# Kernel tuning notes

Hardware: AMD Instinct MI355X
Metric: run time of the kernel (lower is better)

The kernel has to match this reference:

```python
import jax, jax.numpy as jnp
import numpy as np

EVENT_DIM = 128   # event vocabulary
HIDDEN = 256      # 2*128 bilstm output
EMB = 16          # event embedding size
TMP = 128         # tmp_dim
T = 65536         # timesteps
NEG_SLOPE = 0.01  # torch leaky_relu default


def setup_inputs() -> dict:
    key = jax.random.key(0)
    ks = jax.random.split(key, 4)
    return {
        "output": jax.random.normal(ks[0], (T, 1, HIDDEN), dtype=jnp.float32),
        "event_index": 0,  # event_index['NONE']
        "emb_table": jax.random.normal(ks[1], (EVENT_DIM, EMB), dtype=jnp.float32) * 0.02,
        "W1": jax.random.normal(ks[2], (HIDDEN + EMB, TMP), dtype=jnp.float32) / np.sqrt(HIDDEN + EMB).astype(np.float32),
        "b1": jnp.zeros((TMP,), dtype=jnp.float32),
        "W2": jax.random.normal(ks[3], (TMP, EVENT_DIM), dtype=jnp.float32) / np.sqrt(TMP).astype(np.float32),
        "b2": jnp.zeros((EVENT_DIM,), dtype=jnp.float32),
    }


def reference(output, event_index, emb_table, W1, b1, W2, b2):
    # output: [T, 1, HIDDEN]; dropout is identity in eval/inference mode.
    x = output[:, 0, :]  # [T, HIDDEN]

    def step(idx, xt):
        ev = emb_table[idx]                       # [EMB] embedding of previous prediction
        inp = jnp.concatenate([xt, ev], axis=0)   # [HIDDEN+EMB]
        h = jax.nn.leaky_relu(inp @ W1 + b1, negative_slope=NEG_SLOPE)
        logp = jax.nn.log_softmax(h @ W2 + b2)    # [EVENT_DIM]
        nidx = jnp.argmax(logp)                   # greedy feedback (infer=True)
        return nidx, (logp, emb_table[nidx], nidx)

    init = jnp.asarray(event_index, dtype=jnp.int32)
    _, (ner_output, ner_emb, ner_index) = jax.lax.scan(step, init, x)
    # ner_output: [T, EVENT_DIM]; ner_emb: [T, 1, EMB]; ner_index: [T]
    return ner_output, ner_emb[:, None, :], ner_index
```

## Files before the change

### kernel.cpp

```cpp
#include <hip/hip_runtime.h>

#define TT   65536
#define HID  256
#define EMBD 16
#define TMPD 128
#define ED   128
#define TAU  5e-4f
#define EPS  1e-3f
#define NEGINF (-3.402823466e38f)
#define TPB  32
#define CAPW (1u << 20)
#define CMAX 24

typedef __bf16 bf16x8 __attribute__((ext_vector_type(8)));
typedef float  f32x4  __attribute__((ext_vector_type(4)));
typedef short  s16x8  __attribute__((ext_vector_type(8)));

__device__ inline unsigned short f2bf(float f) {
    __bf16 b = (__bf16)f;
    return __builtin_bit_cast(unsigned short, b);
}
__device__ inline float bf2f(unsigned short u) {
    unsigned int x = ((unsigned int)u) << 16;
    return __builtin_bit_cast(float, x);
}
__device__ inline bf16x8 load_frag(const unsigned short* p) {
    uint4 r = *reinterpret_cast<const uint4*>(p);
    return __builtin_bit_cast(bf16x8, r);
}
__device__ inline void split8(const float4& p0, const float4& p1,
                              const float4& e0, const float4& e1,
                              bf16x8& hi, bf16x8& lo)
{
    const float f[8] = {p0.x + e0.x, p0.y + e0.y, p0.z + e0.z, p0.w + e0.w,
                        p1.x + e1.x, p1.y + e1.y, p1.z + e1.z, p1.w + e1.w};
    s16x8 hs, ls;
    #pragma unroll
    for (int q = 0; q < 8; ++q) {
        const float h = fmaxf(f[q], 0.01f * f[q]);
        const unsigned short hb = f2bf(h);
        hs[q] = (short)hb;
        ls[q] = (short)f2bf(h - bf2f(hb));
    }
    hi = __builtin_bit_cast(bf16x8, hs);
    lo = __builtin_bit_cast(bf16x8, ls);
}

__global__ void __launch_bounds__(128) pre_kernel(const float* __restrict__ x,
                                                  const float* __restrict__ W1,
                                                  const float* __restrict__ b1,
                                                  float* __restrict__ pre)
{
    const int j  = threadIdx.x;
    const int t0 = blockIdx.x * 16;

    __shared__ float xs[16 * HID];
    for (int i = j; i < 16 * HID; i += 128)
        xs[i] = x[(size_t)t0 * HID + i];
    __syncthreads();

    double acc[16];
    #pragma unroll
    for (int tt = 0; tt < 16; ++tt) acc[tt] = 0.0;

    #pragma unroll 4
    for (int k = 0; k < HID; ++k) {
        const double w = (double)W1[k * TMPD + j];
        #pragma unroll
        for (int tt = 0; tt < 16; ++tt)
            acc[tt] += (double)xs[tt * HID + k] * w;
    }
    const double bb = (double)b1[j];
    #pragma unroll
    for (int tt = 0; tt < 16; ++tt)
        pre[(size_t)(t0 + tt) * TMPD + j] = (float)(bb + acc[tt]);
}

__global__ void __launch_bounds__(256) w2split_kernel(
    const float* __restrict__ W2,
    unsigned short* __restrict__ W2Th, unsigned short* __restrict__ W2Tl,
    float* __restrict__ W2Tf)
{
    const int gid = blockIdx.x * 256 + threadIdx.x;
    const int k = gid >> 7, j = gid & 127;
    const float v = W2[k * ED + j];
    const unsigned short hi = f2bf(v);
    const unsigned short lo = f2bf(v - bf2f(hi));
    W2Th[j * TMPD + k] = hi;
    W2Tl[j * TMPD + k] = lo;
    W2Tf[j * TMPD + k] = v;
}

__global__ void __launch_bounds__(128) e2z_kernel(
    const float* __restrict__ emb, const float* __restrict__ W1,
    float* __restrict__ E2, float* __restrict__ E2T4,
    unsigned int* __restrict__ meta)
{
    const int i = blockIdx.x;
    const int j = threadIdx.x;
    if (i == 0 && j < 8) meta[j] = 0;
    double a = 0.0;
    #pragma unroll
    for (int m = 0; m < EMBD; ++m)
        a += (double)emb[i * EMBD + m] * (double)W1[(HID + m) * TMPD + j];
    const float v = (float)a;
    E2[i * TMPD + j] = v;
    E2T4[(j >> 2) * 512 + i * 4 + (j & 3)] = v;
}

__global__ void __launch_bounds__(128) dp_kernel(
    const float* __restrict__ E2, const float* __restrict__ W2Tf,
    float* __restrict__ Dp)
{
    const int j = blockIdx.x;
    const int i = threadIdx.x;
    __shared__ float red[2];

    const float* e2r = E2 + (size_t)i * TMPD;
    const float* w2r = W2Tf + (size_t)j * TMPD;
    float s = 0.f;
    #pragma unroll 4
    for (int k = 0; k < TMPD; ++k)
        s = fmaf(fabsf(e2r[k]), fabsf(w2r[k]), s);

    #pragma unroll
    for (int m = 1; m < 64; m <<= 1)
        s = fmaxf(s, __shfl_xor(s, m));
    if ((i & 63) == 0) red[i >> 6] = s;
    __syncthreads();
    if (i == 0) Dp[j] = fmaxf(red[0], red[1]) * 1.0001f + 1e-6f;
}

__global__ void __launch_bounds__(512, 1) l0_kernel(
    const float* __restrict__ pre,
    const unsigned short* __restrict__ W2Th, const unsigned short* __restrict__ W2Tl,
    const float* __restrict__ b2, const float* __restrict__ Dp,
    unsigned char* __restrict__ ftab,
    unsigned char* __restrict__ clist, unsigned char* __restrict__ ccnt,
    unsigned int* __restrict__ tlist, unsigned int* __restrict__ meta)
{
    const int tid = threadIdx.x;
    const int w   = tid >> 6;
    const int l   = tid & 63;
    const int ibase = (w >> 1) * 32;
    const int jhalf = w & 1;
    const int j0    = jhalf * 64;
    const int lc = l & 15, lg = l >> 4;
    const int t0 = blockIdx.x << 7;

    __shared__ float smA [2][128];
    __shared__ int   smAX[2][128];
    __shared__ float smW1[2][128];
    __shared__ int   smWX[2][128];
    __shared__ float smW2[2][128];
    __shared__ unsigned long long smMask[2][128];
    __shared__ float smThr[128];
    __shared__ int   smJ[128];

    bf16x8 Bh[4][4], Bl[4][4];
    #pragma unroll
    for (int jt = 0; jt < 4; ++jt)
        #pragma unroll
        for (int kk = 0; kk < 4; ++kk) {
            const int row = j0 + jt * 16 + lc;
            const int kof = kk * 32 + (lg << 3);
            Bh[jt][kk] = load_frag(W2Th + row * TMPD + kof);
            Bl[jt][kk] = load_frag(W2Tl + row * TMPD + kof);
        }
    float b2v[4], dpv[4];
    #pragma unroll
    for (int jt = 0; jt < 4; ++jt) {
        b2v[jt] = b2[j0 + jt * 16 + lc];
        dpv[jt] = Dp[j0 + jt * 16 + lc];
    }

    f32x4 acc[2][4];
    #pragma unroll
    for (int it = 0; it < 2; ++it)
        #pragma unroll
        for (int jt = 0; jt < 4; ++jt)
            acc[it][jt] = (f32x4){0.f, 0.f, 0.f, 0.f};

    const float4 z4 = {0.f, 0.f, 0.f, 0.f};
    #pragma unroll
    for (int kk = 0; kk < 4; ++kk) {
        const int kof = kk * 32 + (lg << 3);
        bf16x8 Ah[2], Al[2];
        #pragma unroll
        for (int it = 0; it < 2; ++it) {
            const float* pA = pre + (size_t)(t0 + ibase + it * 16 + lc) * TMPD + kof;
            const float4 p0 = *reinterpret_cast<const float4*>(pA);
            const float4 p1 = *reinterpret_cast<const float4*>(pA + 4);
            split8(p0, p1, z4, z4, Ah[it], Al[it]);
        }
        #pragma unroll
        for (int it = 0; it < 2; ++it)
            #pragma unroll
            for (int jt = 0; jt < 4; ++jt) {
                acc[it][jt] = __builtin_amdgcn_mfma_f32_16x16x32_bf16(Al[it], Bh[jt][kk], acc[it][jt], 0, 0, 0);
                acc[it][jt] = __builtin_amdgcn_mfma_f32_16x16x32_bf16(Ah[it], Bl[jt][kk], acc[it][jt], 0, 0, 0);
                acc[it][jt] = __builtin_amdgcn_mfma_f32_16x16x32_bf16(Ah[it], Bh[jt][kk], acc[it][jt], 0, 0, 0);
            }
    }

    #pragma unroll
    for (int it = 0; it < 2; ++it) {
        #pragma unroll
        for (int r = 0; r < 4; ++r) {
            float av0 = acc[it][0][r] + b2v[0];
            float a1 = av0; int x1 = j0 + lc;
            float w1 = av0 + dpv[0]; int wx1 = j0 + lc; float w2 = NEGINF;
            #pragma unroll
            for (int jt = 1; jt < 4; ++jt) {
                const float av = acc[it][jt][r] + b2v[jt];
                const int   jj = j0 + jt * 16 + lc;
                if (av > a1) { a1 = av; x1 = jj; }
                const float wv = av + dpv[jt];
                if (wv > w1) { w2 = w1; w1 = wv; wx1 = jj; }
                else         { w2 = fmaxf(w2, wv); }
            }
            #pragma unroll
            for (int m = 1; m < 16; m <<= 1) {
                const float oa = __shfl_xor(a1, m);
                const int   ox = __shfl_xor(x1, m);
                if (oa > a1 || (oa == a1 && ox < x1)) { a1 = oa; x1 = ox; }
                const float ow1 = __shfl_xor(w1, m);
                const int   owx = __shfl_xor(wx1, m);
                const float ow2 = __shfl_xor(w2, m);
                const bool take = (ow1 > w1) || (ow1 == w1 && owx < wx1);
                const float loser = take ? w1 : ow1;
                w2 = fmaxf(w2, fmaxf(ow2, loser));
                if (take) { w1 = ow1; wx1 = owx; }
            }
            if (lc == 0) {
                const int row = ibase + it * 16 + 4 * lg + r;
                smA [jhalf][row] = a1;  smAX[jhalf][row] = x1;
                smW1[jhalf][row] = w1;  smWX[jhalf][row] = wx1;
                smW2[jhalf][row] = w2;
            }
        }
    }
    __syncthreads();

    if (tid < 128) {
        const int row = tid, t = t0 + row;
        const float A0 = smA[0][row], A1 = smA[1][row];
        const int   X0 = smAX[0][row], X1 = smAX[1][row];
        const bool  h1 = (A1 > A0);
        const float astar = h1 ? A1 : A0;
        const int   jstar = h1 ? X1 : X0;
        const float c0 = (smWX[0][row] == jstar) ? smW2[0][row] : smW1[0][row];
        const float c1 = (smWX[1][row] == jstar) ? smW2[1][row] : smW1[1][row];
        const float M2 = fmaxf(c0, c1);
        const float thr = astar - Dp[jstar] - EPS;
        smJ[row] = jstar;
        if (thr > M2) {
            smThr[row] = 3.0e38f;
            const unsigned int q = (unsigned int)jstar * 0x01010101u;
            const uint4 qv = make_uint4(q, q, q, q);
            uint4* dst = reinterpret_cast<uint4*>(ftab + (size_t)t * ED);
            #pragma unroll
            for (int u = 0; u < 8; ++u) dst[u] = qv;
        } else {
            smThr[row] = thr;
        }
    }
    __syncthreads();

    #pragma unroll
    for (int it = 0; it < 2; ++it) {
        #pragma unroll
        for (int r = 0; r < 4; ++r) {
            const int row = ibase + it * 16 + 4 * lg + r;
            const float thr = smThr[row];
            unsigned long long mask = 0ull;
            #pragma unroll
            for (int jt = 0; jt < 4; ++jt) {
                const float wv = acc[it][jt][r] + b2v[jt] + dpv[jt];
                const unsigned long long b = __ballot(wv >= thr);
                mask |= ((b >> (lg * 16)) & 0xFFFFull) << (jt * 16);
            }
            if (lc == 0) smMask[jhalf][row] = mask;
        }
    }
    __syncthreads();

    if (tid < 128) {
        const int row = tid, t = t0 + row;
        const float thr = smThr[row];
        if (thr < 1e38f) {
            unsigned long long m0 = smMask[0][row], m1 = smMask[1][row];
            const int cnt = __popcll(m0) + __popcll(m1);
            if (cnt > CMAX) {
                ccnt[t] = 0xFFu;
                const unsigned int q = ((unsigned int)smJ[row] | 0x80u) * 0x01010101u;
                const uint4 qv = make_uint4(q, q, q, q);
                uint4* dst = reinterpret_cast<uint4*>(ftab + (size_t)t * ED);
                #pragma unroll
                for (int u = 0; u < 8; ++u) dst[u] = qv;
            } else {
                int c = 0;
                while (m0) { const int b = __ffsll((unsigned long long)m0) - 1;
                             clist[(size_t)t * CMAX + c] = (unsigned char)b; ++c; m0 &= m0 - 1; }
                while (m1) { const int b = __ffsll((unsigned long long)m1) - 1;
                             clist[(size_t)t * CMAX + c] = (unsigned char)(64 + b); ++c; m1 &= m1 - 1; }
                ccnt[t] = (unsigned char)cnt;
                const unsigned int pos = atomicAdd(&meta[1], 1u);
                tlist[pos] = (unsigned int)t;
            }
        }
    }
}

__global__ void __launch_bounds__(128) tier2_kernel(
    const float* __restrict__ pre, const float* __restrict__ E2T4,
    const float* __restrict__ W2Tf, const float* __restrict__ b2,
    const unsigned int* __restrict__ meta,
    const unsigned int* __restrict__ tlist, const unsigned char* __restrict__ ccnt,
    const unsigned char* __restrict__ clist, unsigned char* __restrict__ ftab)
{
    const int i = threadIdx.x;
    __shared__ float Ps[TMPD];
    __shared__ float Ws[8][TMPD];
    __shared__ float vb[8];
    __shared__ unsigned char clj[CMAX];
    __shared__ int scnt;

    const float4* e4p = reinterpret_cast<const float4*>(E2T4) + i;

    const unsigned int n2 = meta[1];
    for (unsigned int u = blockIdx.x; u < n2; u += gridDim.x) {
        const int t = (int)tlist[u];
        if (i == 0) scnt = (int)ccnt[t];
        Ps[i] = pre[(size_t)t * TMPD + i];
        if (i < CMAX) clj[i] = clist[(size_t)t * CMAX + i];
        __syncthreads();
        const int cnt = scnt;

        float t1 = NEGINF, t2 = NEGINF; int x1 = 0;
        for (int g0 = 0; g0 < cnt; g0 += 8) {
            const int gn = min(8, cnt - g0);
            for (int c = 0; c < gn; ++c)
                Ws[c][i] = W2Tf[(int)clj[g0 + c] * TMPD + i];
            if (i < 8) vb[i] = (i < gn) ? b2[clj[g0 + i]] : NEGINF;
            __syncthreads();

            float s[8] = {0.f, 0.f, 0.f, 0.f, 0.f, 0.f, 0.f, 0.f};
            if (gn <= 2) {
                #pragma unroll 4
                for (int kq = 0; kq < 32; ++kq) {
                    const float4 e4 = e4p[kq * ED];
                    const float4 p4 = *reinterpret_cast<const float4*>(&Ps[4 * kq]);
                    const float4 w0 = *reinterpret_cast<const float4*>(&Ws[0][4 * kq]);
                    const float4 w1 = *reinterpret_cast<const float4*>(&Ws[1][4 * kq]);
                    float h;
                    h = p4.x + e4.x; h = fmaxf(h, 0.01f * h);
                    s[0] = fmaf(h, w0.x, s[0]); s[1] = fmaf(h, w1.x, s[1]);
                    h = p4.y + e4.y; h = fmaxf(h, 0.01f * h);
                    s[0] = fmaf(h, w0.y, s[0]); s[1] = fmaf(h, w1.y, s[1]);
                    h = p4.z + e4.z; h = fmaxf(h, 0.01f * h);
                    s[0] = fmaf(h, w0.z, s[0]); s[1] = fmaf(h, w1.z, s[1]);
                    h = p4.w + e4.w; h = fmaxf(h, 0.01f * h);
                    s[0] = fmaf(h, w0.w, s[0]); s[1] = fmaf(h, w1.w, s[1]);
                }
            } else if (gn <= 4) {
                #pragma unroll 2
                for (int kq = 0; kq < 32; ++kq) {
                    const float4 e4 = e4p[kq * ED];
                    const float4 p4 = *reinterpret_cast<const float4*>(&Ps[4 * kq]);
                    const float4 w0 = *reinterpret_cast<const float4*>(&Ws[0][4 * kq]);
                    const float4 w1 = *reinterpret_cast<const float4*>(&Ws[1][4 * kq]);
                    const float4 w2 = *reinterpret_cast<const float4*>(&Ws[2][4 * kq]);
                    const float4 w3 = *reinterpret_cast<const float4*>(&Ws[3][4 * kq]);
                    float h;
                    h = p4.x + e4.x; h = fmaxf(h, 0.01f * h);
                    s[0] = fmaf(h, w0.x, s[0]); s[1] = fmaf(h, w1.x, s[1]);
                    s[2] = fmaf(h, w2.x, s[2]); s[3] = fmaf(h, w3.x, s[3]);
                    h = p4.y + e4.y; h = fmaxf(h, 0.01f * h);
                    s[0] = fmaf(h, w0.y, s[0]); s[1] = fmaf(h, w1.y, s[1]);
                    s[2] = fmaf(h, w2.y, s[2]); s[3] = fmaf(h, w3.y, s[3]);
                    h = p4.z + e4.z; h = fmaxf(h, 0.01f * h);
                    s[0] = fmaf(h, w0.z, s[0]); s[1] = fmaf(h, w1.z, s[1]);
                    s[2] = fmaf(h, w2.z, s[2]); s[3] = fmaf(h, w3.z, s[3]);
                    h = p4.w + e4.w; h = fmaxf(h, 0.01f * h);
                    s[0] = fmaf(h, w0.w, s[0]); s[1] = fmaf(h, w1.w, s[1]);
                    s[2] = fmaf(h, w2.w, s[2]); s[3] = fmaf(h, w3.w, s[3]);
                }
            } else {
                for (int kq = 0; kq < 32; ++kq) {
                    const float4 e4 = e4p[kq * ED];
                    const float4 p4 = *reinterpret_cast<const float4*>(&Ps[4 * kq]);
                    float4 wc[8];
                    #pragma unroll
                    for (int c = 0; c < 8; ++c)
                        wc[c] = *reinterpret_cast<const float4*>(&Ws[c][4 * kq]);
                    float h;
                    h = p4.x + e4.x; h = fmaxf(h, 0.01f * h);
                    #pragma unroll
                    for (int c = 0; c < 8; ++c) s[c] = fmaf(h, wc[c].x, s[c]);
                    h = p4.y + e4.y; h = fmaxf(h, 0.01f * h);
                    #pragma unroll
                    for (int c = 0; c < 8; ++c) s[c] = fmaf(h, wc[c].y, s[c]);
                    h = p4.z + e4.z; h = fmaxf(h, 0.01f * h);
                    #pragma unroll
                    for (int c = 0; c < 8; ++c) s[c] = fmaf(h, wc[c].z, s[c]);
                    h = p4.w + e4.w; h = fmaxf(h, 0.01f * h);
                    #pragma unroll
                    for (int c = 0; c < 8; ++c) s[c] = fmaf(h, wc[c].w, s[c]);
                }
            }

            for (int c = 0; c < gn; ++c) {
                const float v = s[c] + vb[c];
                const int jj = (int)clj[g0 + c];
                if (v > t1) { t2 = t1; t1 = v; x1 = jj; }
                else        { t2 = fmaxf(t2, v); }
            }
            __syncthreads();
        }
        unsigned char byte = (unsigned char)x1;
        if (t1 - t2 < TAU) byte |= 0x80u;
        ftab[(size_t)t * ED + i] = byte;
        __syncthreads();
    }
}

__global__ void __launch_bounds__(256) compact_kernel(
    const unsigned char* __restrict__ ftab,
    unsigned int* __restrict__ meta, unsigned int* __restrict__ work)
{
    const unsigned int gid = blockIdx.x * 256 + threadIdx.x;
    const unsigned int v = reinterpret_cast<const unsigned int*>(ftab)[gid];
    const unsigned int flags = v & 0x80808080u;
    if (flags) {
        const int cnt = __popc(flags);
        unsigned int base = atomicAdd(meta, (unsigned int)cnt);
        #pragma unroll
        for (int b = 0; b < 4; ++b)
            if (v & (0x80u << (8 * b))) {
                if (base < CAPW) work[base] = gid * 4 + b;
                ++base;
            }
    }
}

__global__ void __launch_bounds__(64) repair3_kernel(
    const float* __restrict__ pre, const float* __restrict__ E2,
    const float* __restrict__ W2Tf, const float* __restrict__ b2,
    const unsigned char* __restrict__ clist, const unsigned char* __restrict__ ccnt,
    const unsigned int* __restrict__ meta, const unsigned int* __restrict__ work,
    unsigned char* __restrict__ ftab)
{
    const int l = threadIdx.x;
    unsigned int n = meta[0];
    if (n > CAPW) n = CAPW;

    for (unsigned int u = blockIdx.x; u < n; u += gridDim.x) {
        const unsigned int e = work[u];
        const int t = (int)(e >> 7), i = (int)(e & 127u);

        float h0 = pre[(size_t)t * TMPD + l]      + E2[i * TMPD + l];
        float h1 = pre[(size_t)t * TMPD + 64 + l] + E2[i * TMPD + 64 + l];
        h0 = fmaxf(h0, 0.01f * h0);
        h1 = fmaxf(h1, 0.01f * h1);
        const double H0 = (double)h0, H1 = (double)h1;

        const unsigned char cc = ccnt[t];
        const bool lst = (cc <= (unsigned char)CMAX);
        const int cnt = lst ? (int)cc : 128;

        double best = -1.0e300; int bj = 0;
        for (int c = 0; c < cnt; ++c) {
            const int j = lst ? (int)clist[(size_t)t * CMAX + c] : c;
            const float* wr = W2Tf + (size_t)j * TMPD;
            double s = H0 * (double)wr[l] + H1 * (double)wr[64 + l];
            #pragma unroll
            for (int m = 1; m < 64; m <<= 1)
                s += __shfl_xor(s, m);
            s += (double)b2[j];
            if (s > best) { best = s; bj = j; }
        }
        if (l == 0) ftab[e] = (unsigned char)bj;
    }
}

__global__ void __launch_bounds__(128) repair_kernel(
    const float* __restrict__ pre, const float* __restrict__ E2,
    const float* __restrict__ W2,  const float* __restrict__ b2,
    const unsigned int* __restrict__ meta,
    unsigned char* __restrict__ ftab)
{
    if (meta[0] <= CAPW) return;
    const int j = threadIdx.x;

    __shared__ unsigned char frow[ED];
    __shared__ float  hbuf[TMPD];
    __shared__ double rvd[2];
    __shared__ int    ri[2];

    for (int tt = 0; tt < TPB; ++tt) {
        const int t = blockIdx.x * TPB + tt;
        const unsigned char fb = ftab[(size_t)t * ED + j];
        const int any = __syncthreads_or((int)(fb & 0x80));
        if (!any) continue;

        frow[j] = fb;
        __syncthreads();

        for (int i = 0; i < ED; ++i) {
            if (!(frow[i] & 0x80)) continue;
            const float f = pre[(size_t)t * TMPD + j] + E2[i * TMPD + j];
            hbuf[j] = fmaxf(f, 0.01f * f);
            __syncthreads();
            double a0 = 0.0, a1 = 0.0, a2 = 0.0, a3 = 0.0;
            #pragma unroll
            for (int k = 0; k < TMPD; k += 4) {
                a0 += (double)hbuf[k + 0] * (double)W2[(k + 0) * ED + j];
                a1 += (double)hbuf[k + 1] * (double)W2[(k + 1) * ED + j];
                a2 += (double)hbuf[k + 2] * (double)W2[(k + 2) * ED + j];
                a3 += (double)hbuf[k + 3] * (double)W2[(k + 3) * ED + j];
            }
            double mv = (double)b2[j] + ((a0 + a1) + (a2 + a3));
            int mi = j;
            #pragma unroll
            for (int m = 1; m < 64; m <<= 1) {
                const double ov = __shfl_xor(mv, m);
                const int    oi = __shfl_xor(mi, m);
                if (ov > mv || (ov == mv && oi < mi)) { mv = ov; mi = oi; }
            }
            if ((j & 63) == 0) { rvd[j >> 6] = mv; ri[j >> 6] = mi; }
            __syncthreads();
            int gi;
            if (rvd[1] > rvd[0] || (rvd[1] == rvd[0] && ri[1] < ri[0])) gi = ri[1];
            else gi = ri[0];
            if (j == 0) ftab[(size_t)t * ED + i] = (unsigned char)gi;
            __syncthreads();
        }
        __syncthreads();
    }
}

__global__ void __launch_bounds__(128) walk_kernel(
    const unsigned char* __restrict__ ftab, unsigned char* __restrict__ walk,
    unsigned char* __restrict__ finmap)
{
    const int c   = blockIdx.x;
    const int tid = threadIdx.x;
    __shared__ unsigned char F[512 * 128];

    const uint4* src = reinterpret_cast<const uint4*>(ftab + (size_t)c * 512 * 128);
    uint4* dst = reinterpret_cast<uint4*>(F);
    for (int e = tid; e < 512 * 128 / 16; e += 128) {
        uint4 v = src[e];
        v.x &= 0x7f7f7f7fu; v.y &= 0x7f7f7f7fu; v.z &= 0x7f7f7f7fu; v.w &= 0x7f7f7f7fu;
        dst[e] = v;
    }
    __syncthreads();

    int s = tid;
    unsigned char* wbase = walk + (size_t)c * 512 * 128;
    for (int tt = 0; tt < 512; ++tt) {
        s = F[tt * 128 + s];
        wbase[tt * 128 + tid] = (unsigned char)s;
    }
    finmap[c * 128 + tid] = (unsigned char)s;
}

__global__ void compose_kernel(const unsigned char* __restrict__ finmap,
                               const int* __restrict__ eidx,
                               unsigned char* __restrict__ echain)
{
    if (blockIdx.x == 0 && threadIdx.x == 0) {
        int e = eidx[0];
        for (int c = 0; c < 128; ++c) {
            echain[c] = (unsigned char)e;
            e = finmap[c * 128 + e];
        }
    }
}

__global__ void __launch_bounds__(512, 1) outm_kernel(
    const float* pre, const float* __restrict__ E2,
    const unsigned short* __restrict__ W2Th, const unsigned short* __restrict__ W2Tl,
    const float* __restrict__ b2,
    const unsigned char* __restrict__ walk, const unsigned char* __restrict__ echain,
    const float* __restrict__ emb,
    float* out_logp, float* __restrict__ out_emb, float* __restrict__ out_idx)
{
    const int tid = threadIdx.x;
    const int w   = tid >> 6;
    const int l   = tid & 63;
    const int ibase = (w >> 1) * 32;
    const int jhalf = w & 1;
    const int j0    = jhalf * 64;
    const int lc = l & 15, lg = l >> 4;
    const int t0 = blockIdx.x << 7;
    const int ec = echain[t0 >> 9];

    __shared__ float smM[2][128];
    __shared__ float smS[2][128];
    __shared__ float smLSE[128];

    bf16x8 Bh[4][4], Bl[4][4];
    #pragma unroll
    for (int jt = 0; jt < 4; ++jt)
        #pragma unroll
        for (int kk = 0; kk < 4; ++kk) {
            const int row = j0 + jt * 16 + lc;
            const int kof = kk * 32 + (lg << 3);
            Bh[jt][kk] = load_frag(W2Th + row * TMPD + kof);
            Bl[jt][kk] = load_frag(W2Tl + row * TMPD + kof);
        }
    float b2v[4];
    #pragma unroll
    for (int jt = 0; jt < 4; ++jt) b2v[jt] = b2[j0 + jt * 16 + lc];

    int si[2];
    #pragma unroll
    for (int it = 0; it < 2; ++it) {
        const int t = t0 + ibase + it * 16 + lc;
        si[it] = ((t & 511) == 0) ? ec : (int)walk[(size_t)(t - 1) * 128 + ec];
    }

    f32x4 acc[2][4];
    #pragma unroll
    for (int it = 0; it < 2; ++it)
        #pragma unroll
        for (int jt = 0; jt < 4; ++jt)
            acc[it][jt] = (f32x4){0.f, 0.f, 0.f, 0.f};

    #pragma unroll
    for (int kk = 0; kk < 4; ++kk) {
        const int kof = kk * 32 + (lg << 3);
        bf16x8 Ah[2], Al[2];
        #pragma unroll
        for (int it = 0; it < 2; ++it) {
            const float* pA = pre + (size_t)(t0 + ibase + it * 16 + lc) * TMPD + kof;
            const float* eA = E2 + (size_t)si[it] * TMPD + kof;
            const float4 p0 = *reinterpret_cast<const float4*>(pA);
            const float4 p1 = *reinterpret_cast<const float4*>(pA + 4);
            const float4 e0 = *reinterpret_cast<const float4*>(eA);
            const float4 e1 = *reinterpret_cast<const float4*>(eA + 4);
            split8(p0, p1, e0, e1, Ah[it], Al[it]);
        }
        #pragma unroll
        for (int it = 0; it < 2; ++it)
            #pragma unroll
            for (int jt = 0; jt < 4; ++jt) {
                acc[it][jt] = __builtin_amdgcn_mfma_f32_16x16x32_bf16(Al[it], Bh[jt][kk], acc[it][jt], 0, 0, 0);
                acc[it][jt] = __builtin_amdgcn_mfma_f32_16x16x32_bf16(Ah[it], Bl[jt][kk], acc[it][jt], 0, 0, 0);
                acc[it][jt] = __builtin_amdgcn_mfma_f32_16x16x32_bf16(Ah[it], Bh[jt][kk], acc[it][jt], 0, 0, 0);
            }
    }

    #pragma unroll
    for (int it = 0; it < 2; ++it) {
        #pragma unroll
        for (int r = 0; r < 4; ++r) {
            float v0 = acc[it][0][r] + b2v[0];
            float v1 = acc[it][1][r] + b2v[1];
            float v2 = acc[it][2][r] + b2v[2];
            float v3 = acc[it][3][r] + b2v[3];
            float mx = fmaxf(fmaxf(v0, v1), fmaxf(v2, v3));
            #pragma unroll
            for (int m = 1; m < 16; m <<= 1)
                mx = fmaxf(mx, __shfl_xor(mx, m));
            float s = expf(v0 - mx) + expf(v1 - mx) + expf(v2 - mx) + expf(v3 - mx);
            #pragma unroll
            for (int m = 1; m < 16; m <<= 1)
                s += __shfl_xor(s, m);
            if (lc == 0) {
                const int row = ibase + it * 16 + 4 * lg + r;
                smM[jhalf][row] = mx;
                smS[jhalf][row] = s;
            }
        }
    }
    __syncthreads();

    if (tid < 128) {
        const float m0 = smM[0][tid], m1 = smM[1][tid];
        const float s0 = smS[0][tid], s1 = smS[1][tid];
        const float m = fmaxf(m0, m1);
        smLSE[tid] = m + logf(s0 * expf(m0 - m) + s1 * expf(m1 - m));
    }
    __syncthreads();

    #pragma unroll
    for (int it = 0; it < 2; ++it) {
        #pragma unroll
        for (int r = 0; r < 4; ++r) {
            const int row = ibase + it * 16 + 4 * lg + r;
            const float lse = smLSE[row];
            const int t = t0 + row;
            #pragma unroll
            for (int jt = 0; jt < 4; ++jt)
                out_logp[(size_t)t * TMPD + j0 + jt * 16 + lc] =
                    acc[it][jt][r] + b2v[jt] - lse;
        }
    }

    if (tid < 128) {
        const int t  = t0 + tid;
        const int gi = walk[(size_t)t * 128 + ec];
        out_idx[t] = (float)gi;
        const float4* es = reinterpret_cast<const float4*>(emb + (size_t)gi * EMBD);
        float4*       ed = reinterpret_cast<float4*>(out_emb + (size_t)t * EMBD);
        #pragma unroll
        for (int q = 0; q < 4; ++q) ed[q] = es[q];
    }
}

__global__ void __launch_bounds__(128, 1) seq_kernel(
    const float* pre_in, const int* __restrict__ eidx,
    const float* __restrict__ emb, const float* __restrict__ W1,
    const float* __restrict__ W2, const float* __restrict__ b2,
    float* out_logp, float* __restrict__ out_emb, float* __restrict__ out_idx)
{
    const int j = threadIdx.x;
    __shared__ float  E2s[ED * TMPD];
    __shared__ float  hbuf[TMPD];
    __shared__ double rvd[2];
    __shared__ int    ri[2];
    __shared__ float  rs[2];

    for (int i = 0; i < ED; ++i) {
        double a = 0.0;
        #pragma unroll
        for (int m = 0; m < EMBD; ++m)
            a += (double)emb[i * EMBD + m] * (double)W1[(HID + m) * TMPD + j];
        E2s[i * TMPD + j] = (float)a;
    }
    float w2c[TMPD];
    #pragma unroll 8
    for (int k = 0; k < TMPD; ++k) w2c[k] = W2[k * ED + j];
    const float bias2 = b2[j];
    int idx = eidx[0];
    __syncthreads();

    float pre_cur = pre_in[j];
    for (int t = 0; t < TT; ++t) {
        float pre_next = (t + 1 < TT) ? pre_in[(size_t)(t + 1) * TMPD + j] : 0.0f;
        float h = pre_cur + E2s[idx * TMPD + j];
        h = fmaxf(h, 0.01f * h);
        hbuf[j] = h;
        __syncthreads();
        double a0 = 0, a1 = 0, a2 = 0, a3 = 0;
        #pragma unroll
        for (int k = 0; k < TMPD; k += 4) {
            a0 += (double)hbuf[k + 0] * (double)w2c[k + 0];
            a1 += (double)hbuf[k + 1] * (double)w2c[k + 1];
            a2 += (double)hbuf[k + 2] * (double)w2c[k + 2];
            a3 += (double)hbuf[k + 3] * (double)w2c[k + 3];
        }
        const double logitd = (double)bias2 + ((a0 + a1) + (a2 + a3));
        const float  logit  = (float)logitd;
        double mv = logitd; int mi = j;
        #pragma unroll
        for (int m = 1; m < 64; m <<= 1) {
            double ov = __shfl_xor(mv, m);
            int    oi = __shfl_xor(mi, m);
            if (ov > mv || (ov == mv && oi < mi)) { mv = ov; mi = oi; }
        }
        if ((j & 63) == 0) { rvd[j >> 6] = mv; ri[j >> 6] = mi; }
        __syncthreads();
        int gi; double gmd;
        if (rvd[1] > rvd[0] || (rvd[1] == rvd[0] && ri[1] < ri[0])) { gmd = rvd[1]; gi = ri[1]; }
        else { gmd = rvd[0]; gi = ri[0]; }
        const float gm = (float)gmd;
        float e = expf(logit - gm);
        float s = e;
        #pragma unroll
        for (int m = 1; m < 64; m <<= 1) s += __shfl_xor(s, m);
        if ((j & 63) == 0) rs[j >> 6] = s;
        __syncthreads();
        const float lse = gm + logf(rs[0] + rs[1]);
        out_logp[(size_t)t * TMPD + j] = logit - lse;
        if (j < EMBD) out_emb[(size_t)t * EMBD + j] = emb[gi * EMBD + j];
        if (j == 0)   out_idx[t] = (float)gi;
        idx = gi;
        pre_cur = pre_next;
        __syncthreads();
    }
}

extern "C" void kernel_launch(void* const* d_in, const int* in_sizes, int n_in,
                              void* d_out, int out_size, void* d_ws, size_t ws_size,
                              hipStream_t stream)
{
    const float* x    = (const float*)d_in[0];
    const int*   eidx = (const int*)  d_in[1];
    const float* emb  = (const float*)d_in[2];
    const float* W1   = (const float*)d_in[3];
    const float* b1   = (const float*)d_in[4];
    const float* W2   = (const float*)d_in[5];
    const float* b2   = (const float*)d_in[6];

    float* out0 = (float*)d_out;
    float* out1 = out0 + (size_t)TT * TMPD;
    float* out2 = out1 + (size_t)TT * EMBD;

    const size_t OFF_E2    = 0;
    const size_t OFF_E2T4  = OFF_E2    + 64 * 1024;
    const size_t OFF_W2TH  = OFF_E2T4  + 64 * 1024;
    const size_t OFF_W2TL  = OFF_W2TH  + 32 * 1024;
    const size_t OFF_W2TF  = OFF_W2TL  + 32 * 1024;
    const size_t OFF_DP    = OFF_W2TF  + 64 * 1024;
    const size_t OFF_META  = OFF_DP    + 4 * 1024;
    const size_t OFF_CCNT  = OFF_META  + 4 * 1024;
    const size_t OFF_ECHN  = OFF_CCNT  + 64 * 1024;
    const size_t OFF_FIN   = OFF_ECHN  + 4 * 1024;
    const size_t OFF_TLIST = OFF_FIN   + 16 * 1024;
    const size_t OFF_CLIST = OFF_TLIST + 256 * 1024;
    const size_t OFF_FTAB  = OFF_CLIST + 2048 * 1024;
    const size_t OFF_WALK  = OFF_FTAB  + (size_t)TT * ED;
    const size_t OFF_WORK  = OFF_WALK  + (size_t)TT * ED;
    const size_t AUXN      = OFF_WORK  + (size_t)CAPW * 4;
    const size_t PRE_B     = (size_t)TT * TMPD * sizeof(float);

    unsigned char* wsb = (unsigned char*)d_ws;
    float*          E2    = (float*)(wsb + OFF_E2);
    float*          E2T4  = (float*)(wsb + OFF_E2T4);
    unsigned short* W2Th  = (unsigned short*)(wsb + OFF_W2TH);
    unsigned short* W2Tl  = (unsigned short*)(wsb + OFF_W2TL);
    float*          W2Tf  = (float*)(wsb + OFF_W2TF);
    float*          Dp    = (float*)(wsb + OFF_DP);
    unsigned int*   meta  = (unsigned int*)(wsb + OFF_META);
    unsigned char*  ccnt  = wsb + OFF_CCNT;
    unsigned char*  echn  = wsb + OFF_ECHN;
    unsigned char*  fin   = wsb + OFF_FIN;
    unsigned int*   tlist = (unsigned int*)(wsb + OFF_TLIST);
    unsigned char*  clist = wsb + OFF_CLIST;
    unsigned char*  ftab  = wsb + OFF_FTAB;
    unsigned char*  walk  = wsb + OFF_WALK;
    unsigned int*   work  = (unsigned int*)(wsb + OFF_WORK);

    if (ws_size >= AUXN) {
        float* pre = (ws_size >= AUXN + PRE_B) ? (float*)(wsb + AUXN) : out0;

        pre_kernel    <<<TT / 16,  128, 0, stream>>>(x, W1, b1, pre);
        w2split_kernel<<<64,       256, 0, stream>>>(W2, W2Th, W2Tl, W2Tf);
        e2z_kernel    <<<128,      128, 0, stream>>>(emb, W1, E2, E2T4, meta);
        dp_kernel     <<<128,      128, 0, stream>>>(E2, W2Tf, Dp);
        l0_kernel     <<<TT / 128, 512, 0, stream>>>(pre, W2Th, W2Tl, b2, Dp,
                                                     ftab, clist, ccnt, tlist, meta);
        tier2_kernel  <<<4096,     128, 0, stream>>>(pre, E2T4, W2Tf, b2, meta,
                                                     tlist, ccnt, clist, ftab);
        compact_kernel<<<TT * ED / 4 / 256, 256, 0, stream>>>(ftab, meta, work);
        repair3_kernel<<<8192,      64, 0, stream>>>(pre, E2, W2Tf, b2, clist,
                                                     ccnt, meta, work, ftab);
        repair_kernel <<<TT / TPB, 128, 0, stream>>>(pre, E2, W2, b2, meta, ftab);
        walk_kernel   <<<TT / 512, 128, 0, stream>>>(ftab, walk, fin);
        compose_kernel<<<1,         64, 0, stream>>>(fin, eidx, echn);
        outm_kernel   <<<TT / 128, 512, 0, stream>>>(pre, E2, W2Th, W2Tl, b2,
                                                     walk, echn, emb,
                                                     out0, out1, out2);
    } else {
        float* pre2 = (ws_size >= PRE_B) ? (float*)d_ws : out0;
        pre_kernel<<<TT / 16, 128, 0, stream>>>(x, W1, b1, pre2);
        seq_kernel<<<1, 128, 0, stream>>>(pre2, eidx, emb, W1, W2, b2,
                                          out0, out1, out2);
    }
}
```

Baseline: 445.3 us.

## Compute fp64 input projection with MFMA f64 after runtime layout probe

Replaces the scalar fp64 FMA projection x@W1 with a kernel that uses the fp64 16x16x4 MFMA instruction. W1 is pre-converted to double, x tiles are staged as double in padded LDS, and each wave computes one 16x16 output tile. A one-wave probe kernel works out the MFMA operand and result lane layout at runtime. If no layout matches, a fallback scalar kernel runs. The aim is to cut the cost of the largest dense stage, at the price of three extra launches and a dependency on the probe.

```diff
diff --git a/kernel.cpp b/kernel.cpp
--- a/kernel.cpp
+++ b/kernel.cpp
@@ -11,10 +11,12 @@
 #define TPB  32
 #define CAPW (1u << 20)
 #define CMAX 24
-
-typedef __bf16 bf16x8 __attribute__((ext_vector_type(8)));
-typedef float  f32x4  __attribute__((ext_vector_type(4)));
-typedef short  s16x8  __attribute__((ext_vector_type(8)));
+#define XDP  257
+
+typedef __bf16  bf16x8 __attribute__((ext_vector_type(8)));
+typedef float   f32x4  __attribute__((ext_vector_type(4)));
+typedef short   s16x8  __attribute__((ext_vector_type(8)));
+typedef double  f64x4  __attribute__((ext_vector_type(4)));
 
 __device__ inline unsigned short f2bf(float f) {
     __bf16 b = (__bf16)f;
@@ -46,10 +48,128 @@
     lo = __builtin_bit_cast(bf16x8, ls);
 }
 
-__global__ void __launch_bounds__(128) pre_kernel(const float* __restrict__ x,
-                                                  const float* __restrict__ W1,
-                                                  const float* __restrict__ b1,
-                                                  float* __restrict__ pre)
+__global__ void __launch_bounds__(256) w1d_kernel(const float* __restrict__ W1,
+                                                  double* __restrict__ W1d)
+{
+    const int e = blockIdx.x * 256 + threadIdx.x;
+    W1d[e] = (double)W1[e];
+}
+
+__global__ void __launch_bounds__(64) probe_kernel(unsigned int* __restrict__ pflag)
+{
+    const int l = threadIdx.x;
+    const double a = (double)(l + 1);
+    const double b = (double)(l * l + 3 * l + 7);
+    f64x4 d = {0.0, 0.0, 0.0, 0.0};
+    d = __builtin_amdgcn_mfma_f64_16x16x4f64(a, b, d, 0, 0, 0);
+
+    int found = -1;
+    #pragma unroll
+    for (int c = 0; c < 8; ++c) {
+        const int pA = c & 1, pB = (c >> 1) & 1, pD = (c >> 2) & 1;
+        bool ok = true;
+        #pragma unroll
+        for (int r = 0; r < 4; ++r) {
+            const int m = pD ? (l & 15) : (4 * (l >> 4) + r);
+            const int n = pD ? (4 * (l >> 4) + r) : (l & 15);
+            double exp = 0.0;
+            #pragma unroll
+            for (int k = 0; k < 4; ++k) {
+                const int laneA = pA ? (m * 4 + k) : (m + 16 * k);
+                const int laneB = pB ? (n * 4 + k) : (n + 16 * k);
+                exp += (double)(laneA + 1) *
+                       (double)(laneB * laneB + 3 * laneB + 7);
+            }
+            ok = ok && (d[r] == exp);
+        }
+        const unsigned long long bal = __ballot(ok);
+        if (bal == 0xFFFFFFFFFFFFFFFFull && found < 0) found = c;
+    }
+    if (l == 0) pflag[0] = (found < 0) ? 0xFFu : (unsigned int)found;
+}
+
+__global__ void __launch_bounds__(512) prem_kernel(
+    const float* __restrict__ x, const double* __restrict__ W1d,
+    const float* __restrict__ b1, float* __restrict__ pre,
+    const unsigned int* __restrict__ pflag)
+{
+    const unsigned int c = pflag[0];
+    if (c > 7u) return;
+    const int pA = c & 1, pB = (c >> 1) & 1, pD = (c >> 2) & 1;
+
+    const int tid = threadIdx.x;
+    const int w   = tid >> 6;
+    const int l   = tid & 63;
+    const int t0  = blockIdx.x * 16;
+    const int j0  = w * 16;
+
+    __shared__ double xsd[16 * XDP];
+
+    for (int e = tid; e < 16 * HID; e += 512) {
+        const int tt = e >> 8, k = e & 255;
+        xsd[tt * XDP + k] = (double)x[(size_t)t0 * HID + e];
+    }
+    __syncthreads();
+
+    const int mA = pA ? (l >> 2) : (l & 15);
+    const int kA = pA ? (l & 3)  : (l >> 4);
+    const int nB = pB ? (l >> 2) : (l & 15);
+    const int kB = pB ? (l & 3)  : (l >> 4);
+
+    const double* xrow = xsd + mA * XDP;
+    const double* wcol = W1d + j0 + nB;
+
+    f64x4 acc = {0.0, 0.0, 0.0, 0.0};
+    #pragma unroll 4
+    for (int k0 = 0; k0 < HID; k0 += 4) {
+        const double a = xrow[k0 + kA];
+        const double b = wcol[(size_t)(k0 + kB) * TMPD];
+        acc = __builtin_amdgcn_mfma_f64_16x16x4f64(a, b, acc, 0, 0, 0);
+    }
+    #pragma unroll
+    for (int r = 0; r < 4; ++r) {
+        const int m = pD ? (l & 15) : (4 * (l >> 4) + r);
+        const int n = pD ? (4 * (l >> 4) + r) : (l & 15);
+        pre[(size_t)(t0 + m) * TMPD + j0 + n] =
+            (float)(acc[r] + (double)b1[j0 + n]);
+    }
+}
+
+__global__ void __launch_bounds__(128) prev_kernel(
+    const float* __restrict__ x, const double* __restrict__ W1d,
+    const float* __restrict__ b1, float* __restrict__ pre,
+    const unsigned int* __restrict__ pflag)
+{
+    if (pflag[0] <= 7u) return;
+    const int j  = threadIdx.x;
+    const int t0 = blockIdx.x * 16;
+
+    __shared__ double xsd[16 * XDP];
+    for (int e = j; e < 16 * HID; e += 128)
+        xsd[(e >> 8) * XDP + (e & 255)] = (double)x[(size_t)t0 * HID + e];
+    __syncthreads();
+
+    double acc[16];
+    #pragma unroll
+    for (int tt = 0; tt < 16; ++tt) acc[tt] = 0.0;
+
+    #pragma unroll 2
+    for (int k = 0; k < HID; ++k) {
+        const double w = W1d[(size_t)k * TMPD + j];
+        #pragma unroll
+        for (int tt = 0; tt < 16; ++tt)
+            acc[tt] += xsd[tt * XDP + k] * w;
+    }
+    const double bb = (double)b1[j];
+    #pragma unroll
+    for (int tt = 0; tt < 16; ++tt)
+        pre[(size_t)(t0 + tt) * TMPD + j] = (float)(bb + acc[tt]);
+}
+
+__global__ void __launch_bounds__(128) preold_kernel(const float* __restrict__ x,
+                                                     const float* __restrict__ W1,
+                                                     const float* __restrict__ b1,
+                                                     float* __restrict__ pre)
 {
     const int j  = threadIdx.x;
     const int t0 = blockIdx.x * 16;
@@ -807,7 +927,9 @@
     const size_t OFF_W2TF  = OFF_W2TL  + 32 * 1024;
     const size_t OFF_DP    = OFF_W2TF  + 64 * 1024;
     const size_t OFF_META  = OFF_DP    + 4 * 1024;
-    const size_t OFF_CCNT  = OFF_META  + 4 * 1024;
+    const size_t OFF_FLAG  = OFF_META  + 4 * 1024;
+    const size_t OFF_W1D   = OFF_FLAG  + 4 * 1024;
+    const size_t OFF_CCNT  = OFF_W1D   + 256 * 1024;
     const size_t OFF_ECHN  = OFF_CCNT  + 64 * 1024;
     const size_t OFF_FIN   = OFF_ECHN  + 4 * 1024;
     const size_t OFF_TLIST = OFF_FIN   + 16 * 1024;
@@ -826,6 +948,8 @@
     float*          W2Tf  = (float*)(wsb + OFF_W2TF);
     float*          Dp    = (float*)(wsb + OFF_DP);
     unsigned int*   meta  = (unsigned int*)(wsb + OFF_META);
+    unsigned int*   pflag = (unsigned int*)(wsb + OFF_FLAG);
+    double*         W1d   = (double*)(wsb + OFF_W1D);
     unsigned char*  ccnt  = wsb + OFF_CCNT;
     unsigned char*  echn  = wsb + OFF_ECHN;
     unsigned char*  fin   = wsb + OFF_FIN;
@@ -838,7 +962,10 @@
     if (ws_size >= AUXN) {
         float* pre = (ws_size >= AUXN + PRE_B) ? (float*)(wsb + AUXN) : out0;
 
-        pre_kernel    <<<TT / 16,  128, 0, stream>>>(x, W1, b1, pre);
+        w1d_kernel    <<<128,      256, 0, stream>>>(W1, W1d);
+        probe_kernel  <<<1,         64, 0, stream>>>(pflag);
+        prem_kernel   <<<TT / 16,  512, 0, stream>>>(x, W1d, b1, pre, pflag);
+        prev_kernel   <<<TT / 16,  128, 0, stream>>>(x, W1d, b1, pre, pflag);
         w2split_kernel<<<64,       256, 0, stream>>>(W2, W2Th, W2Tl, W2Tf);
         e2z_kernel    <<<128,      128, 0, stream>>>(emb, W1, E2, E2T4, meta);
         dp_kernel     <<<128,      128, 0, stream>>>(E2, W2Tf, Dp);
@@ -857,7 +984,7 @@
                                                      out0, out1, out2);
     } else {
         float* pre2 = (ws_size >= PRE_B) ? (float*)d_ws : out0;
-        pre_kernel<<<TT / 16, 128, 0, stream>>>(x, W1, b1, pre2);
+        preold_kernel<<<TT / 16, 128, 0, stream>>>(x, W1, b1, pre2);
         seq_kernel<<<1, 128, 0, stream>>>(pre2, eidx, emb, W1, W2, b2,
                                           out0, out1, out2);
     }
```

Result: slower. 533.6 us (+19.8%).
